# Performance work log

Measured on AMD Instinct MI355X. Metric: run time of the kernel, lower is better.

The kernel has to match this reference:

```python
import jax, jax.numpy as jnp
import numpy as np

EMBED_DIM = 1024
NUM_HEADS = 16
HEAD_DIM = EMBED_DIM // NUM_HEADS
ROPE_BASE = 10000.0


def rotate_half(x):
    # interleaved variant: pairs (x0,x1) -> (-x1, x0)
    x1 = x[..., ::2]
    x2 = x[..., 1::2]
    return jnp.stack((-x2, x1), axis=-1).reshape(x.shape)


def rope_tables(T, dim, dtype):
    inv_freq = 1.0 / (ROPE_BASE ** (jnp.arange(0, dim, 2, dtype=jnp.float32) / dim))
    t = jnp.arange(T, dtype=jnp.float32)
    freqs = t[:, None] * inv_freq[None, :]          # [T, dim/2]
    emb = jnp.concatenate((freqs, freqs), axis=-1)  # [T, dim]
    return jnp.cos(emb).astype(dtype), jnp.sin(emb).astype(dtype)


def setup_inputs() -> dict:
    key = jax.random.key(0)
    kx, kq, ko = jax.random.split(key, 3)
    B, T, D = 2, 2048, EMBED_DIM
    x = jax.random.normal(kx, (B, T, D), dtype=jnp.float32)
    s = 1.0 / np.sqrt(D)
    Wqkv = jax.random.normal(kq, (D, 3 * D), dtype=jnp.float32) * s
    Wout = jax.random.normal(ko, (D, D), dtype=jnp.float32) * s
    return {"x": x, "Wqkv": Wqkv, "Wout": Wout}


def reference(x, Wqkv, Wout):
    B, T, D = x.shape
    H, hd = NUM_HEADS, HEAD_DIM
    qkv = x @ Wqkv                                   # [B,T,3D]
    q, k, v = jnp.split(qkv, 3, axis=-1)
    q = q.reshape(B, T, H, hd).transpose(0, 2, 1, 3)  # [B,H,T,hd]
    k = k.reshape(B, T, H, hd).transpose(0, 2, 1, 3)
    v = v.reshape(B, T, H, hd).transpose(0, 2, 1, 3)
    cos, sin = rope_tables(T, hd, x.dtype)           # [T,hd]
    cos = cos[None, None, :, :]
    sin = sin[None, None, :, :]
    q = q * cos + rotate_half(q) * sin
    k = k * cos + rotate_half(k) * sin
    scale = 1.0 / np.sqrt(hd).astype(np.float32)
    attn = jnp.einsum('bhtd,bhsd->bhts', q, k) * scale  # [B,H,T,T]
    attn = jax.nn.softmax(attn, axis=-1)
    out = jnp.einsum('bhts,bhsd->bhtd', attn, v)     # [B,H,T,hd]
    out = out.transpose(0, 2, 1, 3).reshape(B, T, D)
    return out @ Wout
```

## Files before the change

kernel.cpp:

```cpp
#include <hip/hip_runtime.h>
#include <hip/hip_bf16.h>
#include <stdint.h>


typedef unsigned short u16;
typedef short bf16x8 __attribute__((ext_vector_type(8)));
typedef float f32x4  __attribute__((ext_vector_type(4)));
typedef float f32x16 __attribute__((ext_vector_type(16)));

#if defined(__has_builtin) && __has_builtin(__builtin_amdgcn_exp2f)
#define EXP2F(x) __builtin_amdgcn_exp2f(x)
#else
#define EXP2F(x) exp2f(x)
#endif

__device__ __forceinline__ u16 f2b(float f) {
  uint32_t u = __float_as_uint(f);
  u += 0x7fffu + ((u >> 16) & 1u);
  return (u16)(u >> 16);
}
__device__ __forceinline__ uint32_t pkbf(float a, float b) {
  __hip_bfloat162 h = __float22bfloat162_rn(make_float2(a, b));
  union { __hip_bfloat162 h2; uint32_t u; } cv; cv.h2 = h;
  return cv.u;
}

__device__ __forceinline__ void gl2lds16(const void* g, void* l) {
  __builtin_amdgcn_global_load_lds(
      (const __attribute__((address_space(1))) unsigned int*)g,
      (__attribute__((address_space(3))) unsigned int*)l, 16, 0, 0);
}

__device__ __forceinline__ int sniff_x(const void* x, int tid, int* sh) {
  const u16* xu = (const u16*)x;
  if (tid == 0) *sh = 0;
  __syncthreads();
  int c = 0;
  #pragma unroll
  for (int i = 0; i < 16; i++) {
    const int idx = tid + i * 256;
    float a = fabsf(__uint_as_float(((uint32_t)xu[2 * idx]) << 16));
    if (a > 1e-3f && a < 100.f) c++;
  }
  c += __shfl_down(c, 32, 64);
  c += __shfl_down(c, 16, 64);
  c += __shfl_down(c, 8, 64);
  c += __shfl_down(c, 4, 64);
  c += __shfl_down(c, 2, 64);
  c += __shfl_down(c, 1, 64);
  if ((tid & 63) == 0) atomicAdd(sh, c);
  __syncthreads();
  return (*sh > 2048) ? 1 : 0;
}

__device__ __forceinline__ void tr_tile(const void* src, u16* dst, int Kd, int N,
                                        int n0, int k0, int isb, u16* Lt, int tid)
{
  const int r = tid >> 2, cseg = (tid & 3) << 4;
  u16 t[16];
  if (isb) {
    const u16* s = (const u16*)src + (size_t)(k0 + r) * N + n0 + cseg;
    *(uint4*)&t[0] = *(const uint4*)s;
    *(uint4*)&t[8] = *(const uint4*)(s + 8);
  } else {
    const float* s = (const float*)src + (size_t)(k0 + r) * N + n0 + cseg;
    #pragma unroll
    for (int j = 0; j < 4; j++) {
      float4 v = *(const float4*)(s + j * 4);
      t[j*4+0] = f2b(v.x); t[j*4+1] = f2b(v.y); t[j*4+2] = f2b(v.z); t[j*4+3] = f2b(v.w);
    }
  }
  #pragma unroll
  for (int j = 0; j < 16; j++) Lt[(cseg + j) * 72 + r] = t[j];
  __syncthreads();
  const int n = tid >> 2, kseg = (tid & 3) << 4;
  uint4 u0 = *(const uint4*)&Lt[n * 72 + kseg];
  uint4 u1 = *(const uint4*)&Lt[n * 72 + kseg + 8];
  u16* d = dst + (size_t)(n0 + n) * Kd + k0 + kseg;
  *(uint4*)d = u0;
  *(uint4*)(d + 8) = u1;
}

__global__ __launch_bounds__(256) void prep_kernel(
    const void* __restrict__ x, const void* __restrict__ wqkv,
    const void* __restrict__ wout, int xbf,
    u16* __restrict__ Xb, u16* __restrict__ Wqkvt, u16* __restrict__ Woutt,
    float2* __restrict__ CS)
{
  __shared__ u16 Lt[64 * 72];
  __shared__ int snf;
  const int bid = blockIdx.x, tid = threadIdx.x;
  if (bid < 2048) {
    if (xbf) return;
    const int isb = sniff_x(x, tid, &snf);
    const size_t i = ((size_t)bid * 256 + tid) * 8;
    if (isb) {
      *(uint4*)&Xb[i] = *(const uint4*)((const u16*)x + i);
    } else {
      const float* s = (const float*)x + i;
      float4 a = *(const float4*)s, b = *(const float4*)(s + 4);
      uint4 p;
      p.x = pkbf(a.x, a.y); p.y = pkbf(a.z, a.w);
      p.z = pkbf(b.x, b.y); p.w = pkbf(b.z, b.w);
      *(uint4*)&Xb[i] = p;
    }
  } else if (bid < 2816) {
    const int isb = sniff_x(x, tid, &snf);
    const int b = bid - 2048;
    tr_tile(wqkv, Wqkvt, 1024, 3072, (b % 48) * 64, (b / 48) * 64, isb, Lt, tid);
  } else if (bid < 3072) {
    const int isb = sniff_x(x, tid, &snf);
    const int b = bid - 2816;
    tr_tile(wout, Woutt, 1024, 1024, (b % 16) * 64, (b / 16) * 64, isb, Lt, tid);
  } else {
    const int idx = (bid - 3072) * 256 + tid;
    const int t = idx >> 5, f = idx & 31;
    float invf = __expf(-(float)f * 0.2878231366242557f);
    float th = (float)t * invf;
    float sn, cs;
    sincosf(th, &sn, &cs);
    CS[idx] = make_float2(cs, sn);
  }
}

__global__ __launch_bounds__(256) void qkv_kernel(
    const u16* __restrict__ Asrc, const u16* __restrict__ Wt,
    const float2* __restrict__ CS,
    u16* __restrict__ Q, u16* __restrict__ K, u16* __restrict__ Vt)
{
  __shared__ u16 As[128 * 64];
  __shared__ u16 Bs[128 * 64];
  const int tid = threadIdx.x;
  const int bidx = blockIdx.x;
  const int swz = (bidx & 7) * 96 + (bidx >> 3);
  const int n0 = (swz % 24) * 128;
  const int m0 = (swz / 24) * 128;
  const int w = tid >> 6, l = tid & 63, lr = l & 15, lq = l >> 4;
  const int mrow0 = (w & 1) * 64;
  const int ncol0 = (w >> 1) * 64;
  const int srow = tid >> 3;
  const int gseg = (tid & 7) ^ (srow & 7);

  const int col0 = n0 + ncol0;
  const int sec = col0 >> 10;
  const int isv = (sec == 2);
  const int h = (col0 >> 6) & 15;

  f32x4 acc[4][4] = {};

  for (int k0 = 0; k0 < 1024; k0 += 64) {
    __syncthreads();
    #pragma unroll
    for (int rd = 0; rd < 4; rd++) {
      const int row = srow + rd * 32;
      gl2lds16(Asrc + (size_t)(m0 + row) * 1024 + k0 + gseg * 8, &As[tid * 8 + rd * 2048]);
      gl2lds16(Wt + (size_t)(n0 + row) * 1024 + k0 + gseg * 8, &Bs[tid * 8 + rd * 2048]);
    }
    __syncthreads();
    #pragma unroll
    for (int kc = 0; kc < 2; kc++) {
      bf16x8 af[4], bf[4];
      #pragma unroll
      for (int i = 0; i < 4; i++) {
        const int seg = ((kc << 2) | lq) ^ (lr & 7);
        af[i] = *(const bf16x8*)&As[(mrow0 + i * 16 + lr) * 64 + seg * 8];
        bf[i] = *(const bf16x8*)&Bs[(ncol0 + i * 16 + lr) * 64 + seg * 8];
      }
      if (isv) {
        #pragma unroll
        for (int mb = 0; mb < 4; mb++)
          #pragma unroll
          for (int nb = 0; nb < 4; nb++)
            acc[mb][nb] = __builtin_amdgcn_mfma_f32_16x16x32_bf16(af[mb], bf[nb], acc[mb][nb], 0, 0, 0);
      } else {
        #pragma unroll
        for (int mb = 0; mb < 4; mb++)
          #pragma unroll
          for (int nb = 0; nb < 4; nb++)
            acc[mb][nb] = __builtin_amdgcn_mfma_f32_16x16x32_bf16(bf[nb], af[mb], acc[mb][nb], 0, 0, 0);
      }
    }
  }

  if (isv) {
    #pragma unroll
    for (int mb = 0; mb < 4; mb++) {
      const int row0 = m0 + mrow0 + mb * 16 + lq * 4;
      const int b = row0 >> 11, t0 = row0 & 2047;
      const int tp = (t0 & ~12) | ((t0 & 4) << 1) | ((t0 & 8) >> 1);
      #pragma unroll
      for (int nb = 0; nb < 4; nb++) {
        const int d = nb * 16 + lr;
        uint2 uv;
        uv.x = pkbf(acc[mb][nb][0], acc[mb][nb][1]);
        uv.y = pkbf(acc[mb][nb][2], acc[mb][nb][3]);
        *(uint2*)&Vt[(((size_t)b * 16 + h) * 64 + d) * 2048 + tp] = uv;
      }
    }
  } else {
    u16* dst = (sec == 0) ? Q : K;
    const float qscale = 0.125f * 1.44269504f;
    #pragma unroll
    for (int mb = 0; mb < 4; mb++) {
      const int m = m0 + mrow0 + mb * 16 + lr;
      const int b = m >> 11, t = m & 2047;
      const float* csrow = (const float*)(CS + t * 32);
      #pragma unroll
      for (int nb = 0; nb < 4; nb++) {
        const int d = nb * 16 + lq * 4;
        const int fb = d & 31;
        f32x4 c01 = *(const f32x4*)(csrow + 2 * fb);
        f32x4 c23 = *(const f32x4*)(csrow + 2 * fb + 4);
        float v0 = acc[mb][nb][0], v1 = acc[mb][nb][1];
        float v2 = acc[mb][nb][2], v3 = acc[mb][nb][3];
        float r0 = v0 * c01[0] - v1 * c01[1];
        float r1 = fmaf(v1, c01[2], v0 * c01[3]);
        float r2 = v2 * c23[0] - v3 * c23[1];
        float r3 = fmaf(v3, c23[2], v2 * c23[3]);
        if (sec == 0) { r0 *= qscale; r1 *= qscale; r2 *= qscale; r3 *= qscale; }
        uint2 uv;
        uv.x = pkbf(r0, r1);
        uv.y = pkbf(r2, r3);
        *(uint2*)&dst[(((size_t)b * 16 + h) * 2048 + t) * 64 + d] = uv;
      }
    }
  }
}

__global__ __launch_bounds__(512, 4) void attn_kernel(
    const u16* __restrict__ Q, const u16* __restrict__ K,
    const u16* __restrict__ Vt, u16* __restrict__ ATT)
{
  __shared__ u16 pool[2][2][2][4096];
  const int tid = threadIdx.x;
  const int shard = tid >> 8;
  const int t2 = tid & 255;
  const int ws = (tid >> 6) & 3;
  const int l = tid & 63;
  const int m5 = l & 31, hi = l >> 5;

  const int bid = blockIdx.x;
  const int swz = (bid & 7) * 64 + (bid >> 3);
  const int bh = swz >> 4;
  const int qt = swz & 15;

  const int sbeg = shard * 1024;
  const size_t base = (size_t)bh * (2048 * 64);
  const int qrow0 = qt * 128 + ws * 32;
  const int t_own = qrow0 + m5;

  bf16x8 qf[4];
  #pragma unroll
  for (int kd = 0; kd < 4; kd++)
    qf[kd] = *(const bf16x8*)(Q + base + (size_t)t_own * 64 + kd * 16 + hi * 8);

  f32x16 oa[2] = {};
  float lsum = 0.f;

  const int srow = t2 >> 3;

  auto stage = [&](int buf, int s0) {
    #pragma unroll
    for (int rd = 0; rd < 2; rd++) {
      const int row = srow + rd * 32;
      const int gs = (t2 & 7) ^ (row & 7) ^ ((row >> 3) & 3);
      gl2lds16(K + base + (size_t)(s0 + row) * 64 + gs * 8,
               &pool[shard][0][buf][t2 * 8 + rd * 2048]);
      gl2lds16(Vt + base + (size_t)row * 2048 + s0 + gs * 8,
               &pool[shard][1][buf][t2 * 8 + rd * 2048]);
    }
  };

  stage(0, sbeg);
  const int nt = 16;

  #pragma unroll 1
  for (int t = 0; t < nt; t++) {
    const int buf = t & 1;
    __syncthreads();
    if (t + 1 < nt) stage(buf ^ 1, sbeg + (t + 1) * 64);
    const u16* Ks = pool[shard][0][buf];
    const u16* Vs = pool[shard][1][buf];

    uint32_t pw[2][8];
    #pragma unroll
    for (int sb = 0; sb < 2; sb++) {
      const int row = sb * 32 + m5;
      const int sw = (row & 7) ^ ((row >> 3) & 3);
      bf16x8 kf[4];
      #pragma unroll
      for (int kd = 0; kd < 4; kd++)
        kf[kd] = *(const bf16x8*)&Ks[row * 64 + ((((kd << 1) | hi) ^ sw) << 3)];
      f32x16 z = {};
      __builtin_amdgcn_s_setprio(1);
      z = __builtin_amdgcn_mfma_f32_32x32x16_bf16(kf[0], qf[0], z, 0, 0, 0);
      z = __builtin_amdgcn_mfma_f32_32x32x16_bf16(kf[1], qf[1], z, 0, 0, 0);
      z = __builtin_amdgcn_mfma_f32_32x32x16_bf16(kf[2], qf[2], z, 0, 0, 0);
      z = __builtin_amdgcn_mfma_f32_32x32x16_bf16(kf[3], qf[3], z, 0, 0, 0);
      __builtin_amdgcn_s_setprio(0);
      float e[16];
      #pragma unroll
      for (int r = 0; r < 16; r++) e[r] = EXP2F(z[r]);
      lsum += (((e[0] + e[1]) + (e[2] + e[3])) + ((e[4] + e[5]) + (e[6] + e[7])))
            + (((e[8] + e[9]) + (e[10] + e[11])) + ((e[12] + e[13]) + (e[14] + e[15])));
      #pragma unroll
      for (int w2 = 0; w2 < 8; w2++)
        pw[sb][w2] = pkbf(e[2 * w2], e[2 * w2 + 1]);
    }

    #pragma unroll
    for (int db = 0; db < 2; db++) {
      const int row = db * 32 + m5;
      const int sw = (row & 7) ^ ((row >> 3) & 3);
      bf16x8 vf[4];
      #pragma unroll
      for (int sblk = 0; sblk < 4; sblk++)
        vf[sblk] = *(const bf16x8*)&Vs[row * 64 + ((((sblk << 1) | hi) ^ sw) << 3)];
      __builtin_amdgcn_s_setprio(1);
      #pragma unroll
      for (int sblk = 0; sblk < 4; sblk++) {
        union { uint32_t u[4]; bf16x8 v; } pf;
        const int sb = sblk >> 1, off = (sblk & 1) * 4;
        pf.u[0] = pw[sb][off + 0]; pf.u[1] = pw[sb][off + 1];
        pf.u[2] = pw[sb][off + 2]; pf.u[3] = pw[sb][off + 3];
        oa[db] = __builtin_amdgcn_mfma_f32_32x32x16_bf16(vf[sblk], pf.v, oa[db], 0, 0, 0);
      }
      __builtin_amdgcn_s_setprio(0);
    }
  }

  lsum += __shfl_xor(lsum, 32, 64);

  float* mo = (float*)pool;
  __syncthreads();
  if (shard == 1) {
    #pragma unroll
    for (int db = 0; db < 2; db++)
      #pragma unroll
      for (int r = 0; r < 16; r++)
        mo[((ws * 32 + db * 16 + r) << 6) + l] = oa[db][r];
    mo[8192 + ws * 64 + l] = lsum;
  }
  __syncthreads();
  if (shard == 0) {
    const float ls2 = mo[8192 + ws * 64 + l];
    const float inv = 1.f / (lsum + ls2);
    const int b = bh >> 4, h = bh & 15;
    u16* dst = ATT + ((size_t)(b * 2048 + t_own)) * 1024 + h * 64;
    #pragma unroll
    for (int db = 0; db < 2; db++)
      #pragma unroll
      for (int rq = 0; rq < 4; rq++) {
        const int d0 = db * 32 + rq * 8 + hi * 4;
        float s0 = oa[db][4 * rq + 0] + mo[((ws * 32 + db * 16 + 4 * rq + 0) << 6) + l];
        float s1 = oa[db][4 * rq + 1] + mo[((ws * 32 + db * 16 + 4 * rq + 1) << 6) + l];
        float s2 = oa[db][4 * rq + 2] + mo[((ws * 32 + db * 16 + 4 * rq + 2) << 6) + l];
        float s3 = oa[db][4 * rq + 3] + mo[((ws * 32 + db * 16 + 4 * rq + 3) << 6) + l];
        uint2 u;
        u.x = pkbf(s0 * inv, s1 * inv);
        u.y = pkbf(s2 * inv, s3 * inv);
        *(uint2*)&dst[d0] = u;
      }
  }
}

__global__ __launch_bounds__(256) void outproj_kernel(
    const u16* __restrict__ A, const u16* __restrict__ Wt,
    const void* __restrict__ xprobe, void* __restrict__ outv)
{
  __shared__ u16 As[128 * 64];
  __shared__ u16 Bs[128 * 64];
  __shared__ int snf;
  const int tid = threadIdx.x;
  const int isb = sniff_x(xprobe, tid, &snf);
  const int bidx = blockIdx.x;
  const int n0 = (bidx & 7) * 128;
  const int m0 = (bidx >> 3) * 128;
  const int w = tid >> 6, l = tid & 63, lr = l & 15, lq = l >> 4;
  const int mrow0 = (w & 1) * 64;
  const int ncol0 = (w >> 1) * 64;
  const int srow = tid >> 3;
  const int gseg = (tid & 7) ^ (srow & 7);

  f32x4 acc[4][4] = {};

  for (int k0 = 0; k0 < 1024; k0 += 64) {
    __syncthreads();
    #pragma unroll
    for (int rd = 0; rd < 4; rd++) {
      const int row = srow + rd * 32;
      gl2lds16(A + (size_t)(m0 + row) * 1024 + k0 + gseg * 8, &As[tid * 8 + rd * 2048]);
      gl2lds16(Wt + (size_t)(n0 + row) * 1024 + k0 + gseg * 8, &Bs[tid * 8 + rd * 2048]);
    }
    __syncthreads();
    #pragma unroll
    for (int kc = 0; kc < 2; kc++) {
      bf16x8 af[4], bf[4];
      #pragma unroll
      for (int i = 0; i < 4; i++) {
        const int seg = ((kc << 2) | lq) ^ (lr & 7);
        af[i] = *(const bf16x8*)&As[(mrow0 + i * 16 + lr) * 64 + seg * 8];
        bf[i] = *(const bf16x8*)&Bs[(ncol0 + i * 16 + lr) * 64 + seg * 8];
      }
      #pragma unroll
      for (int mb = 0; mb < 4; mb++)
        #pragma unroll
        for (int nb = 0; nb < 4; nb++)
          acc[mb][nb] = __builtin_amdgcn_mfma_f32_16x16x32_bf16(bf[nb], af[mb], acc[mb][nb], 0, 0, 0);
    }
  }
  #pragma unroll
  for (int mb = 0; mb < 4; mb++) {
    const int row = m0 + mrow0 + mb * 16 + lr;
    #pragma unroll
    for (int nb = 0; nb < 4; nb++) {
      const int col = n0 + ncol0 + nb * 16 + lq * 4;
      f32x4 v = acc[mb][nb];
      if (isb) {
        uint2 uv;
        uv.x = pkbf(v[0], v[1]);
        uv.y = pkbf(v[2], v[3]);
        *(uint2*)&((u16*)outv)[(size_t)row * 1024 + col] = uv;
      } else {
        *(f32x4*)&((float*)outv)[(size_t)row * 1024 + col] = v;
      }
    }
  }
}

extern "C" void kernel_launch(void* const* d_in, const int* in_sizes, int n_in,
                              void* d_out, int out_size, void* d_ws, size_t ws_size,
                              hipStream_t stream)
{
  const void* x    = d_in[0];
  const void* wqkv = d_in[1];
  const void* wout = d_in[2];
  char* ws = (char*)d_ws;
  const size_t MB = 1024 * 1024;
  float2* CS     = (float2*)(ws + 1024);
  u16*    Xb     = (u16*)(ws + 1 * MB);
  u16*    ATT    = Xb;
  u16*    Wqkvt  = (u16*)(ws + 9 * MB);
  u16*    Woutt  = (u16*)(ws + 15 * MB);
  u16*    Q      = (u16*)(ws + 17 * MB);
  u16*    K      = (u16*)(ws + 25 * MB);
  u16*    Vt     = (u16*)(ws + 33 * MB);

  const int xbf = (in_sizes && in_sizes[0] == 8388608) ? 1 : 0;
  const u16* Asrc = xbf ? (const u16*)x : Xb;

  prep_kernel<<<3328, 256, 0, stream>>>(x, wqkv, wout, xbf, Xb, Wqkvt, Woutt, CS);
  qkv_kernel<<<dim3(768), 256, 0, stream>>>(Asrc, Wqkvt, CS, Q, K, Vt);
  attn_kernel<<<dim3(512), 512, 0, stream>>>(Q, K, Vt, ATT);
  outproj_kernel<<<dim3(256), 256, 0, stream>>>(ATT, Woutt, x, d_out);
}
```

Baseline: 194.6 us.

## Double-buffer LDS tiles in QKV and out-projection GEMMs with one barrier per step

Both GEMM kernels now keep two LDS buffers and use a K step of 32 instead of 64. The next tile's global-to-LDS copy is issued before computing on the current buffer, with one barrier per iteration instead of two. A new XOR swizzle matches the 32-wide rows. This aims to hide load latency behind MFMA work, at the cost of twice as many loop iterations and less work per barrier.

```diff
diff --git a/kernel.cpp b/kernel.cpp
--- a/kernel.cpp
+++ b/kernel.cpp
@@ -128,8 +128,8 @@
     const float2* __restrict__ CS,
     u16* __restrict__ Q, u16* __restrict__ K, u16* __restrict__ Vt)
 {
-  __shared__ u16 As[128 * 64];
-  __shared__ u16 Bs[128 * 64];
+  __shared__ u16 As[2][4096];
+  __shared__ u16 Bs[2][4096];
   const int tid = threadIdx.x;
   const int bidx = blockIdx.x;
   const int swz = (bidx & 7) * 96 + (bidx >> 3);
@@ -138,47 +138,52 @@
   const int w = tid >> 6, l = tid & 63, lr = l & 15, lq = l >> 4;
   const int mrow0 = (w & 1) * 64;
   const int ncol0 = (w >> 1) * 64;
-  const int srow = tid >> 3;
-  const int gseg = (tid & 7) ^ (srow & 7);
 
   const int col0 = n0 + ncol0;
   const int sec = col0 >> 10;
   const int isv = (sec == 2);
   const int h = (col0 >> 6) & 15;
 
+  const int srow = tid >> 2;
+  const int ss0 = (tid & 3) ^ ((srow >> 1) & 3);
+  const int ss1 = (tid & 3) ^ (((srow + 64) >> 1) & 3);
+
+  auto stageq = [&](int buf, int k0) {
+    gl2lds16(Asrc + (size_t)(m0 + srow) * 1024 + k0 + ss0 * 8, &As[buf][tid * 8]);
+    gl2lds16(Wt   + (size_t)(n0 + srow) * 1024 + k0 + ss0 * 8, &Bs[buf][tid * 8]);
+    gl2lds16(Asrc + (size_t)(m0 + 64 + srow) * 1024 + k0 + ss1 * 8, &As[buf][2048 + tid * 8]);
+    gl2lds16(Wt   + (size_t)(n0 + 64 + srow) * 1024 + k0 + ss1 * 8, &Bs[buf][2048 + tid * 8]);
+  };
+
   f32x4 acc[4][4] = {};
-
-  for (int k0 = 0; k0 < 1024; k0 += 64) {
+  const int fsw = (lr >> 1) & 3;
+
+  stageq(0, 0);
+  #pragma unroll 1
+  for (int t = 0; t < 32; t++) {
+    const int buf = t & 1;
     __syncthreads();
-    #pragma unroll
-    for (int rd = 0; rd < 4; rd++) {
-      const int row = srow + rd * 32;
-      gl2lds16(Asrc + (size_t)(m0 + row) * 1024 + k0 + gseg * 8, &As[tid * 8 + rd * 2048]);
-      gl2lds16(Wt + (size_t)(n0 + row) * 1024 + k0 + gseg * 8, &Bs[tid * 8 + rd * 2048]);
-    }
-    __syncthreads();
-    #pragma unroll
-    for (int kc = 0; kc < 2; kc++) {
-      bf16x8 af[4], bf[4];
-      #pragma unroll
-      for (int i = 0; i < 4; i++) {
-        const int seg = ((kc << 2) | lq) ^ (lr & 7);
-        af[i] = *(const bf16x8*)&As[(mrow0 + i * 16 + lr) * 64 + seg * 8];
-        bf[i] = *(const bf16x8*)&Bs[(ncol0 + i * 16 + lr) * 64 + seg * 8];
-      }
-      if (isv) {
+    if (t + 1 < 32) stageq(buf ^ 1, (t + 1) * 32);
+    bf16x8 af[4], bf[4];
+    #pragma unroll
+    for (int i = 0; i < 4; i++) {
+      const int ra = mrow0 + i * 16 + lr;
+      const int rb = ncol0 + i * 16 + lr;
+      af[i] = *(const bf16x8*)&As[buf][ra * 32 + ((lq ^ fsw) << 3)];
+      bf[i] = *(const bf16x8*)&Bs[buf][rb * 32 + ((lq ^ fsw) << 3)];
+    }
+    if (isv) {
+      #pragma unroll
+      for (int mb = 0; mb < 4; mb++)
         #pragma unroll
-        for (int mb = 0; mb < 4; mb++)
-          #pragma unroll
-          for (int nb = 0; nb < 4; nb++)
-            acc[mb][nb] = __builtin_amdgcn_mfma_f32_16x16x32_bf16(af[mb], bf[nb], acc[mb][nb], 0, 0, 0);
-      } else {
+        for (int nb = 0; nb < 4; nb++)
+          acc[mb][nb] = __builtin_amdgcn_mfma_f32_16x16x32_bf16(af[mb], bf[nb], acc[mb][nb], 0, 0, 0);
+    } else {
+      #pragma unroll
+      for (int mb = 0; mb < 4; mb++)
         #pragma unroll
-        for (int mb = 0; mb < 4; mb++)
-          #pragma unroll
-          for (int nb = 0; nb < 4; nb++)
-            acc[mb][nb] = __builtin_amdgcn_mfma_f32_16x16x32_bf16(bf[nb], af[mb], acc[mb][nb], 0, 0, 0);
-      }
+        for (int nb = 0; nb < 4; nb++)
+          acc[mb][nb] = __builtin_amdgcn_mfma_f32_16x16x32_bf16(bf[nb], af[mb], acc[mb][nb], 0, 0, 0);
     }
   }
 
@@ -368,8 +373,8 @@
     const u16* __restrict__ A, const u16* __restrict__ Wt,
     const void* __restrict__ xprobe, void* __restrict__ outv)
 {
-  __shared__ u16 As[128 * 64];
-  __shared__ u16 Bs[128 * 64];
+  __shared__ u16 As[2][4096];
+  __shared__ u16 Bs[2][4096];
   __shared__ int snf;
   const int tid = threadIdx.x;
   const int isb = sniff_x(xprobe, tid, &snf);
@@ -379,36 +384,42 @@
   const int w = tid >> 6, l = tid & 63, lr = l & 15, lq = l >> 4;
   const int mrow0 = (w & 1) * 64;
   const int ncol0 = (w >> 1) * 64;
-  const int srow = tid >> 3;
-  const int gseg = (tid & 7) ^ (srow & 7);
+
+  const int srow = tid >> 2;
+  const int ss0 = (tid & 3) ^ ((srow >> 1) & 3);
+  const int ss1 = (tid & 3) ^ (((srow + 64) >> 1) & 3);
+
+  auto stageq = [&](int buf, int k0) {
+    gl2lds16(A  + (size_t)(m0 + srow) * 1024 + k0 + ss0 * 8, &As[buf][tid * 8]);
+    gl2lds16(Wt + (size_t)(n0 + srow) * 1024 + k0 + ss0 * 8, &Bs[buf][tid * 8]);
+    gl2lds16(A  + (size_t)(m0 + 64 + srow) * 1024 + k0 + ss1 * 8, &As[buf][2048 + tid * 8]);
+    gl2lds16(Wt + (size_t)(n0 + 64 + srow) * 1024 + k0 + ss1 * 8, &Bs[buf][2048 + tid * 8]);
+  };
 
   f32x4 acc[4][4] = {};
-
-  for (int k0 = 0; k0 < 1024; k0 += 64) {
+  const int fsw = (lr >> 1) & 3;
+
+  stageq(0, 0);
+  #pragma unroll 1
+  for (int t = 0; t < 32; t++) {
+    const int buf = t & 1;
     __syncthreads();
-    #pragma unroll
-    for (int rd = 0; rd < 4; rd++) {
-      const int row = srow + rd * 32;
-      gl2lds16(A + (size_t)(m0 + row) * 1024 + k0 + gseg * 8, &As[tid * 8 + rd * 2048]);
-      gl2lds16(Wt + (size_t)(n0 + row) * 1024 + k0 + gseg * 8, &Bs[tid * 8 + rd * 2048]);
-    }
-    __syncthreads();
-    #pragma unroll
-    for (int kc = 0; kc < 2; kc++) {
-      bf16x8 af[4], bf[4];
-      #pragma unroll
-      for (int i = 0; i < 4; i++) {
-        const int seg = ((kc << 2) | lq) ^ (lr & 7);
-        af[i] = *(const bf16x8*)&As[(mrow0 + i * 16 + lr) * 64 + seg * 8];
-        bf[i] = *(const bf16x8*)&Bs[(ncol0 + i * 16 + lr) * 64 + seg * 8];
-      }
-      #pragma unroll
-      for (int mb = 0; mb < 4; mb++)
-        #pragma unroll
-        for (int nb = 0; nb < 4; nb++)
-          acc[mb][nb] = __builtin_amdgcn_mfma_f32_16x16x32_bf16(bf[nb], af[mb], acc[mb][nb], 0, 0, 0);
-    }
-  }
+    if (t + 1 < 32) stageq(buf ^ 1, (t + 1) * 32);
+    bf16x8 af[4], bf[4];
+    #pragma unroll
+    for (int i = 0; i < 4; i++) {
+      const int ra = mrow0 + i * 16 + lr;
+      const int rb = ncol0 + i * 16 + lr;
+      af[i] = *(const bf16x8*)&As[buf][ra * 32 + ((lq ^ fsw) << 3)];
+      bf[i] = *(const bf16x8*)&Bs[buf][rb * 32 + ((lq ^ fsw) << 3)];
+    }
+    #pragma unroll
+    for (int mb = 0; mb < 4; mb++)
+      #pragma unroll
+      for (int nb = 0; nb < 4; nb++)
+        acc[mb][nb] = __builtin_amdgcn_mfma_f32_16x16x32_bf16(bf[nb], af[mb], acc[mb][nb], 0, 0, 0);
+  }
+
   #pragma unroll
   for (int mb = 0; mb < 4; mb++) {
     const int row = m0 + mrow0 + mb * 16 + lr;
```

Result: slower. 202.7 us (+4.2%).
